# Optimization experiments

Hardware: AMD Instinct MI355X
Metric: run time of the kernel (lower is better)

The kernel has to match this reference:

```python
import jax, jax.numpy as jnp
import numpy as np

DIM = 256
RADIUS = 3
DIAM = 2 * RADIUS + 1          # 7
NNEIGH = DIAM * DIAM           # 49
B, H, W = 2, 64, 64
EPS_LN = 1e-6
EPS_NORM = 1e-7


def conv1x1(x, w, b):
    # x: [B,Cin,H,W], w: [Cout,Cin], b: [Cout]
    return jnp.einsum('oi,bihw->bohw', w, x) + b[None, :, None, None]


def layernorm2d(x, g, b):
    # channel-wise norm as in LayerNorm2d (mean/var over channel dim)
    u = x.mean(1, keepdims=True)
    s = ((x - u) ** 2).mean(1, keepdims=True)
    xn = (x - u) / jnp.sqrt(s + EPS_LN)
    return g[None, :, None, None] * xn + b[None, :, None, None]


def unfold_reflect(x, r):
    # torch F.unfold(pad(x, reflect, r), kernel=2r+1).reshape(B,C,D*D,H,W)
    d = 2 * r + 1
    hh, ww = x.shape[2], x.shape[3]
    xp = jnp.pad(x, ((0, 0), (0, 0), (r, r), (r, r)), mode='reflect')
    pats = [xp[:, :, i:i + hh, j:j + ww] for i in range(d) for j in range(d)]
    return jnp.stack(pats, axis=2)  # [B,C,D*D,H,W]


def setup_inputs() -> dict:
    key = jax.random.key(0)
    ks = jax.random.split(key, 20)
    sc_c = 1.0 / np.sqrt(DIM)
    sc_f = 1.0 / np.sqrt(NNEIGH + DIM)
    inp = {
        'spatial_feats': jax.random.normal(ks[0], (B, DIM, H, W), jnp.float32),
        'semantic_feats': jax.random.normal(ks[1], (B, DIM, H, W), jnp.float32),
        # range_proj: conv1x1 -> LN2d -> SiLU -> conv1x1
        'rp_w1': jax.random.normal(ks[2], (DIM, DIM), jnp.float32) * sc_c,
        'rp_b1': jnp.zeros((DIM,), jnp.float32),
        'rp_g': jnp.ones((DIM,), jnp.float32),
        'rp_be': jnp.zeros((DIM,), jnp.float32),
        'rp_w2': jax.random.normal(ks[3], (DIM, DIM), jnp.float32) * sc_c,
        'rp_b2': jnp.zeros((DIM,), jnp.float32),
        # fixup_proj: conv1x1(49+C->49) -> LN2d -> SiLU -> conv1x1(49->49)
        'fp_w1': jax.random.normal(ks[4], (NNEIGH, NNEIGH + DIM), jnp.float32) * sc_f,
        'fp_b1': jnp.zeros((NNEIGH,), jnp.float32),
        'fp_g': jnp.ones((NNEIGH,), jnp.float32),
        'fp_be': jnp.zeros((NNEIGH,), jnp.float32),
        'fp_w2': jax.random.normal(ks[5], (NNEIGH, NNEIGH), jnp.float32) * (1.0 / np.sqrt(NNEIGH)),
        'fp_b2': jnp.zeros((NNEIGH,), jnp.float32),
        # output_proj: conv1x1 -> LN2d -> conv1x1
        'op_w1': jax.random.normal(ks[6], (DIM, DIM), jnp.float32) * sc_c,
        'op_b1': jnp.zeros((DIM,), jnp.float32),
        'op_g': jnp.ones((DIM,), jnp.float32),
        'op_be': jnp.zeros((DIM,), jnp.float32),
        'op_w2': jax.random.normal(ks[7], (DIM, DIM), jnp.float32) * sc_c,
        'op_b2': jnp.zeros((DIM,), jnp.float32),
        'sigma_spatial': jnp.ones((), jnp.float32),
    }
    return inp


def reference(spatial_feats, semantic_feats,
              rp_w1, rp_b1, rp_g, rp_be, rp_w2, rp_b2,
              fp_w1, fp_b1, fp_g, fp_be, fp_w2, fp_b2,
              op_w1, op_b1, op_g, op_be, op_w2, op_b2,
              sigma_spatial):
    scale = jnp.asarray(DIM ** 0.5, spatial_feats.dtype)
    # range_proj(semantic_feats)
    px = conv1x1(semantic_feats, rp_w1, rp_b1)
    px = jax.nn.silu(layernorm2d(px, rp_g, rp_be))
    px = conv1x1(px, rp_w2, rp_b2)  # [B,C,H,W]

    # spatial (Gaussian) kernel over the window
    lin = jnp.linspace(-1.0, 1.0, DIAM)
    xg, yg = jnp.meshgrid(lin, lin, indexing='ij')
    spatial_kernel = jnp.exp(-(xg ** 2 + yg ** 2) / (2.0 * sigma_spatial ** 2))
    spatial_kernel = spatial_kernel.reshape(1, NNEIGH, 1, 1)

    # range kernel: local similarity + softmax over the 49 neighbors
    queries = unfold_reflect(px, RADIUS)                       # [B,C,N,H,W]
    sim = jnp.einsum('bcnhw,bchw->bnhw', queries, px) / scale
    range_kernel = jax.nn.softmax(sim.astype(jnp.float32), axis=1).astype(px.dtype)

    # neighborhoods of spatial features
    neighborhoods = unfold_reflect(spatial_feats, RADIUS)      # [B,C,N,H,W]

    # gated fixup correction
    ck = range_kernel * spatial_kernel                          # [B,N,H,W]
    fx = conv1x1(jnp.concatenate([ck, semantic_feats], axis=1), fp_w1, fp_b1)
    fx = jax.nn.silu(layernorm2d(fx, fp_g, fp_be))
    fx = conv1x1(fx, fp_w2, fp_b2)
    ck = ck + ck * jax.nn.sigmoid(fx)
    ck = ck / (ck.sum(1, keepdims=True) + EPS_NORM)

    # weighted neighborhood sum
    out = jnp.einsum('bcnhw,bnhw->bchw', neighborhoods, ck)

    # output_proj (note: no SiLU here, matching the module)
    out = conv1x1(out, op_w1, op_b1)
    out = layernorm2d(out, op_g, op_be)
    out = conv1x1(out, op_w2, op_b2)
    return out
```

## Files before the change

kernel.cpp:

```cpp
#include <hip/hip_runtime.h>
#include <cstdint>

#define HW 4096
#define C_ 256
#define NN 49
#define KW 305

typedef __bf16 bf16;
typedef bf16 bf16x8 __attribute__((ext_vector_type(8)));
typedef bf16 bf16x4 __attribute__((ext_vector_type(4)));
typedef float f32x4 __attribute__((ext_vector_type(4)));

#define GLD16(src, dst) __builtin_amdgcn_global_load_lds( \
    (const __attribute__((address_space(1))) uint32_t*)(src), \
    (__attribute__((address_space(3))) uint32_t*)(dst), 16, 0, 0)

__device__ __forceinline__ int refl(int i) { return i < 0 ? -i : (i > 63 ? 126 - i : i); }
__device__ __forceinline__ float sigmoidf_(float x) { return 1.f / (1.f + __expf(-x)); }

__global__ __launch_bounds__(256) void setup_k(const float* __restrict__ spatial,
                                               const float* __restrict__ semantic,
                                               const float* __restrict__ rp_w1,
                                               const float* __restrict__ rp_w2,
                                               const float* __restrict__ op_w1,
                                               const float* __restrict__ op_w2,
                                               const float* __restrict__ fp_w1,
                                               const float* __restrict__ fp_w2,
                                               const float* __restrict__ sigma,
                                               bf16* __restrict__ spb, bf16* __restrict__ seb,
                                               bf16* __restrict__ wrp1, bf16* __restrict__ wrp2,
                                               bf16* __restrict__ wop1, bf16* __restrict__ wop2,
                                               bf16* __restrict__ w1ckb, bf16* __restrict__ w1sb,
                                               bf16* __restrict__ w2Tg, float* __restrict__ sk)
{
    __shared__ float tile[32][33];
    const int bid = blockIdx.x, t = threadIdx.x;
    if (bid < 4096) {
        int z = bid >> 10, r = bid & 1023;
        int b = z & 1;
        const float* src = (z >> 1) ? semantic : spatial;
        bf16* dst = (z >> 1) ? seb : spb;
        int p0 = (r & 127) * 32, c0 = (r >> 7) * 32;
        int tx = t & 31, ty = t >> 5;
        const float* s = src + (size_t)b * C_ * HW;
        #pragma unroll
        for (int i = 0; i < 32; i += 8)
            tile[ty + i][tx] = s[(size_t)(c0 + ty + i) * HW + p0 + tx];
        __syncthreads();
        int p = t >> 3, cq = (t & 7) * 4;
        bf16x4 o = {(bf16)tile[cq][p], (bf16)tile[cq + 1][p], (bf16)tile[cq + 2][p], (bf16)tile[cq + 3][p]};
        *(bf16x4*)&dst[((size_t)b * HW + p0 + p) * C_ + c0 + cq] = o;
        return;
    }
    int pid = bid - 4096;
    if (pid < 256) {
        const float* src = (pid < 64) ? rp_w1 : (pid < 128) ? rp_w2 : (pid < 192) ? op_w1 : op_w2;
        bf16* dst = (pid < 64) ? wrp1 : (pid < 128) ? wrp2 : (pid < 192) ? wop1 : wop2;
        int i = ((pid & 63) * 256 + t) * 4;
        f32x4 v = *(const f32x4*)&src[i];
        bf16x4 o = {(bf16)v[0], (bf16)v[1], (bf16)v[2], (bf16)v[3]};
        *(bf16x4*)&dst[i] = o;
    } else if (pid == 256) {
        if (t < NN) {
            int i = t / 7, j = t % 7;
            float xg = (i - 3) * (1.f / 3.f), yg = (j - 3) * (1.f / 3.f);
            float s = sigma[0];
            sk[t] = __expf(-(xg * xg + yg * yg) / (2.f * s * s));
        }
    } else if (pid < 270) {
        int idx = (pid - 257) * 256 + t;
        if (idx < NN * 64) {
            int k = idx >> 6, o = idx & 63;
            w1ckb[idx] = (o < NN) ? (bf16)fp_w1[o * KW + k] : (bf16)0.f;
        }
    } else if (pid < 334) {
        int idx = (pid - 270) * 256 + t;
        int o = idx >> 8, c = idx & 255;
        w1sb[idx] = (o < NN) ? (bf16)fp_w1[o * KW + NN + c] : (bf16)0.f;
    } else {
        int idx = (pid - 334) * 256 + t;
        if (idx < NN * 64) {
            int k = idx >> 6, o = idx & 63;
            w2Tg[idx] = (o < NN) ? (bf16)fp_w2[o * NN + k] : (bf16)0.f;
        }
    }
}

__device__ __forceinline__ void stage_b(const bf16* __restrict__ Wp, bf16* dst, int kc, int t)
{
    const bf16* gB = Wp + (size_t)(t >> 2) * C_ + kc + (((t & 3) ^ ((t >> 3) & 3)) * 8);
    #pragma unroll
    for (int ii = 0; ii < 4; ++ii)
        GLD16(gB + (size_t)ii * 64 * C_, dst + ii * 2048 + t * 8);
}

template<bool SILU, int MODE>
__global__ __launch_bounds__(256) void conv_pair(const bf16* __restrict__ X,
                                                 const bf16* __restrict__ W1,
                                                 const float* __restrict__ b1v,
                                                 const float* __restrict__ g,
                                                 const float* __restrict__ be,
                                                 const bf16* __restrict__ W2,
                                                 const float* __restrict__ b2v,
                                                 void* __restrict__ Yv)
{
    __shared__ __align__(16) bf16 Xf[32 * 256];
    __shared__ __align__(16) bf16 Mid[32 * 256];
    __shared__ __align__(16) bf16 Bs[2][256 * 32];
    __shared__ float lnred[32][4][2];
    const int t = threadIdx.x;
    const int lane = t & 63, wc = t >> 6;
    const int l15 = lane & 15, kb = lane >> 4;
    const long q0 = (long)blockIdx.x * 32;

    {
        const int r8 = t >> 5, slot = t & 31;
        const bf16* gX = X + (q0 + r8) * C_ + ((slot ^ (r8 & 7)) * 8);
        #pragma unroll
        for (int i = 0; i < 4; ++i)
            GLD16(gX + (size_t)i * 8 * C_, &Xf[i * 2048 + t * 8]);
    }
    stage_b(W1, &Bs[0][0], 0, t);

    const int x7 = l15 & 7;
    const int bsl = (kb ^ ((l15 >> 1) & 3)) * 8;
    int boff[4];
    #pragma unroll
    for (int n = 0; n < 4; ++n)
        boff[n] = (wc * 64 + n * 16 + l15) * 32 + bsl;
    const int a0base = l15 * 256;
    const int a1base = (16 + l15) * 256;

    f32x4 acc[2][4];
    #pragma unroll
    for (int m = 0; m < 2; ++m)
        #pragma unroll
        for (int n = 0; n < 4; ++n) acc[m][n] = (f32x4){0.f, 0.f, 0.f, 0.f};

    __syncthreads();
    int cur = 0;
    #pragma unroll
    for (int ks = 0; ks < 8; ++ks) {
        if (ks < 7) stage_b(W1, &Bs[cur ^ 1][0], (ks + 1) * 32, t);
        const int ko = ((ks * 4 + kb) ^ x7) * 8;
        bf16x8 a0 = *(const bf16x8*)&Xf[a0base + ko];
        bf16x8 a1 = *(const bf16x8*)&Xf[a1base + ko];
        #pragma unroll
        for (int n = 0; n < 4; ++n) {
            bf16x8 b = *(const bf16x8*)&Bs[cur][boff[n]];
            acc[0][n] = __builtin_amdgcn_mfma_f32_16x16x32_bf16(a0, b, acc[0][n], 0, 0, 0);
            acc[1][n] = __builtin_amdgcn_mfma_f32_16x16x32_bf16(a1, b, acc[1][n], 0, 0, 0);
        }
        __syncthreads();
        cur ^= 1;
    }

    stage_b(W2, &Bs[0][0], 0, t);

    float s4[2][4], ss4[2][4];
    #pragma unroll
    for (int m = 0; m < 2; ++m)
        #pragma unroll
        for (int r = 0; r < 4; ++r) { s4[m][r] = 0.f; ss4[m][r] = 0.f; }
    #pragma unroll
    for (int n = 0; n < 4; ++n) {
        float bo = b1v[wc * 64 + n * 16 + l15];
        #pragma unroll
        for (int m = 0; m < 2; ++m)
            #pragma unroll
            for (int r = 0; r < 4; ++r) {
                float v = acc[m][n][r] + bo;
                acc[m][n][r] = v;
                s4[m][r] += v; ss4[m][r] += v * v;
            }
    }
    #pragma unroll
    for (int off = 1; off <= 8; off <<= 1)
        #pragma unroll
        for (int m = 0; m < 2; ++m)
            #pragma unroll
            for (int r = 0; r < 4; ++r) {
                s4[m][r]  += __shfl_xor(s4[m][r], off, 64);
                ss4[m][r] += __shfl_xor(ss4[m][r], off, 64);
            }
    if (l15 == 0) {
        #pragma unroll
        for (int m = 0; m < 2; ++m)
            #pragma unroll
            for (int r = 0; r < 4; ++r) {
                lnred[m * 16 + kb * 4 + r][wc][0] = s4[m][r];
                lnred[m * 16 + kb * 4 + r][wc][1] = ss4[m][r];
            }
    }
    __syncthreads();
    float mean[2][4], rstd[2][4];
    #pragma unroll
    for (int m = 0; m < 2; ++m)
        #pragma unroll
        for (int r = 0; r < 4; ++r) {
            int p = m * 16 + kb * 4 + r;
            float st  = lnred[p][0][0] + lnred[p][1][0] + lnred[p][2][0] + lnred[p][3][0];
            float sst = lnred[p][0][1] + lnred[p][1][1] + lnred[p][2][1] + lnred[p][3][1];
            mean[m][r] = st * (1.f / 256.f);
            float var = sst * (1.f / 256.f) - mean[m][r] * mean[m][r];
            rstd[m][r] = rsqrtf(var + 1e-6f);
        }
    #pragma unroll
    for (int n = 0; n < 4; ++n) {
        int ch = wc * 64 + n * 16 + l15;
        float gv = g[ch], bev = be[ch];
        #pragma unroll
        for (int m = 0; m < 2; ++m)
            #pragma unroll
            for (int r = 0; r < 4; ++r) {
                float y = (acc[m][n][r] - mean[m][r]) * rstd[m][r] * gv + bev;
                if (SILU) y *= sigmoidf_(y);
                int p = m * 16 + kb * 4 + r;
                Mid[p * 256 + (((ch >> 3) ^ (p & 7)) * 8) + (ch & 7)] = (bf16)y;
            }
    }
    __syncthreads();

    f32x4 acc2[2][4];
    #pragma unroll
    for (int m = 0; m < 2; ++m)
        #pragma unroll
        for (int n = 0; n < 4; ++n) acc2[m][n] = (f32x4){0.f, 0.f, 0.f, 0.f};
    cur = 0;
    #pragma unroll
    for (int ks = 0; ks < 8; ++ks) {
        if (ks < 7) stage_b(W2, &Bs[cur ^ 1][0], (ks + 1) * 32, t);
        const int ko = ((ks * 4 + kb) ^ x7) * 8;
        bf16x8 a0 = *(const bf16x8*)&Mid[a0base + ko];
        bf16x8 a1 = *(const bf16x8*)&Mid[a1base + ko];
        #pragma unroll
        for (int n = 0; n < 4; ++n) {
            bf16x8 b = *(const bf16x8*)&Bs[cur][boff[n]];
            acc2[0][n] = __builtin_amdgcn_mfma_f32_16x16x32_bf16(a0, b, acc2[0][n], 0, 0, 0);
            acc2[1][n] = __builtin_amdgcn_mfma_f32_16x16x32_bf16(a1, b, acc2[1][n], 0, 0, 0);
        }
        __syncthreads();
        cur ^= 1;
    }

    if constexpr (MODE == 0) {
        #pragma unroll
        for (int n = 0; n < 4; ++n) {
            int ch = wc * 64 + n * 16 + l15;
            float bo = b2v[ch];
            #pragma unroll
            for (int m = 0; m < 2; ++m)
                #pragma unroll
                for (int r = 0; r < 4; ++r)
                    Xf[(m * 16 + kb * 4 + r) * 256 + ch] = (bf16)(acc2[m][n][r] + bo);
        }
        __syncthreads();
        bf16* Y = (bf16*)Yv;
        const int p = t >> 3, cb = (t & 7) * 32;
        #pragma unroll
        for (int i = 0; i < 4; ++i) {
            bf16x8 v = *(const bf16x8*)&Xf[p * 256 + cb + i * 8];
            *(bf16x8*)&Y[(q0 + p) * C_ + cb + i * 8] = v;
        }
    } else {
        float* Y = (float*)Yv;
        const int bb = (int)(q0 >> 12);
        #pragma unroll
        for (int n = 0; n < 4; ++n) {
            int ch = wc * 64 + n * 16 + l15;
            float bo = b2v[ch];
            #pragma unroll
            for (int m = 0; m < 2; ++m) {
                int pp = (int)(q0 & 4095) + m * 16 + kb * 4;
                f32x4 val = {acc2[m][n][0] + bo, acc2[m][n][1] + bo,
                             acc2[m][n][2] + bo, acc2[m][n][3] + bo};
                *(f32x4*)&Y[((size_t)bb * C_ + ch) * HW + pp] = val;
            }
        }
    }
}

__global__ __launch_bounds__(256) void attn_out_k(const bf16* __restrict__ px,
                                                  const bf16* __restrict__ spb,
                                                  const bf16* __restrict__ seb,
                                                  const bf16* __restrict__ w1sb,
                                                  const bf16* __restrict__ w1ckb,
                                                  const bf16* __restrict__ w2Tg,
                                                  const float* __restrict__ b1,
                                                  const float* __restrict__ b2,
                                                  const float* __restrict__ g,
                                                  const float* __restrict__ be,
                                                  const float* __restrict__ sk,
                                                  const bf16* __restrict__ wop1,
                                                  const float* __restrict__ ob1,
                                                  const float* __restrict__ og,
                                                  const float* __restrict__ obe,
                                                  const bf16* __restrict__ wop2,
                                                  const float* __restrict__ ob2,
                                                  float* __restrict__ Y)
{
    __shared__ __align__(16) char shm[72768];
    bf16*  uni = (bf16*)(shm);
    float* ckl = (float*)(shm + 51200);
    float* hb  = (float*)(shm + 55360);
    float* S   = (float*)(shm + 56384);
    float* fxs = (float*)(shm + 64000);
    bf16*  Bs0 = (bf16*)(shm + 56384);
    bf16*  Bs1 = (bf16*)(shm + 16384);
    bf16*  Xg  = (bf16*)(shm);
    bf16*  Mid = (bf16*)(shm + 32768);
    float* lnred = (float*)(shm + 40960);

    const int t = threadIdx.x, lane = t & 63, wid = t >> 6;
    const int l15 = lane & 15, kb = lane >> 4, l31 = lane & 31;
    const int blk = blockIdx.x;
    const int batch = blk >> 8, tt = blk & 255;
    const int h0 = (tt >> 4) * 4, w0 = (tt & 15) * 4;
    const long base = (long)batch * HW;

    const float bo  = (lane < NN) ? b1[lane] : 0.f;
    const float gl  = (lane < NN) ? g[lane] : 0.f;
    const float bel = (lane < NN) ? be[lane] : 0.f;
    const float b2l = (lane < NN) ? b2[lane] : 0.f;
    const float skv = (lane < NN) ? sk[lane] : 0.f;
    const int nn_ = (lane < NN) ? lane : 0;
    const int dy = nn_ / 7, dx = nn_ % 7;

    #pragma unroll
    for (int i = 0; i < 13; ++i) {
        int st = i * 256 + t;
        if (st < 3200) {
            int u = st >> 5, s = st & 31;
            int uy = (u * 205) >> 11, ux = u - uy * 10;
            long grow = base + refl(h0 + uy - 3) * 64 + refl(w0 + ux - 3);
            GLD16(spb + grow * C_ + s * 8, &uni[u * 256 + s * 8]);
        }
    }

    const int ppy = l15 >> 2, ppx = l15 & 3;
    const long qB = base + (h0 + ppy) * 64 + (w0 + ppx);
    const bf16* bpxp = px + qB * C_ + kb * 8;
    const bf16* bsemp = seb + qB * C_ + kb * 8;

    bool valid[3], ispx[3];
    const bf16* arow[3];
    #pragma unroll
    for (int j = 0; j < 3; ++j) {
        int tid = wid + 4 * j;
        valid[j] = tid < 11;
        ispx[j] = tid < 7;
        int u = tid * 16 + l15;
        int uy = (u * 205) >> 11, ux = u - uy * 10;
        long grow = (u < 100) ? base + refl(h0 + uy - 3) * 64 + refl(w0 + ux - 3) : base;
        int o = ((tid - 7) & 3) * 16 + l15;
        arow[j] = ispx[j] ? (px + grow * C_ + kb * 8)
                          : (w1sb + (size_t)o * C_ + kb * 8);
    }

    f32x4 acc[3];
    #pragma unroll
    for (int j = 0; j < 3; ++j) acc[j] = (f32x4){0.f, 0.f, 0.f, 0.f};

    #pragma unroll
    for (int ks = 0; ks < 8; ++ks) {
        bf16x8 bp = *(const bf16x8*)(bpxp + ks * 32);
        bf16x8 bs = *(const bf16x8*)(bsemp + ks * 32);
        #pragma unroll
        for (int j = 0; j < 3; ++j) {
            if (valid[j]) {
                bf16x8 a = *(const bf16x8*)(arow[j] + ks * 32);
                acc[j] = __builtin_amdgcn_mfma_f32_16x16x32_bf16(a, ispx[j] ? bp : bs, acc[j], 0, 0, 0);
            }
        }
    }

    float w1r[NN], w2r[NN];
    #pragma unroll
    for (int k = 0; k < NN; ++k) {
        w1r[k] = (float)w1ckb[k * 64 + lane];
        w2r[k] = (float)w2Tg[k * 64 + lane];
    }

    #pragma unroll
    for (int j = 0; j < 3; ++j) {
        if (valid[j]) {
            int tid = wid + 4 * j;
            float* dst = ispx[j] ? &S[(tid * 16 + kb * 4) * 17 + l15]
                                 : &fxs[(((tid - 7) * 16) + kb * 4) * 17 + l15];
            dst[0] = acc[j][0]; dst[17] = acc[j][1]; dst[34] = acc[j][2]; dst[51] = acc[j][3];
        }
    }
    __syncthreads();

    #pragma unroll
    for (int j = 0; j < 4; ++j) {
        int p = wid * 4 + j, py = p >> 2, px4 = p & 3;
        int u = (py + dy) * 10 + px4 + dx;
        float sval = (lane < NN) ? S[u * 17 + p] * 0.0625f : -1e30f;
        float mx = sval;
        #pragma unroll
        for (int off = 32; off; off >>= 1) mx = fmaxf(mx, __shfl_xor(mx, off, 64));
        float ev = (lane < NN) ? __expf(sval - mx) : 0.f;
        float ssum = ev;
        #pragma unroll
        for (int off = 32; off; off >>= 1) ssum += __shfl_xor(ssum, off, 64);
        ckl[p * 65 + lane] = (lane < NN) ? (ev / ssum) * skv : 0.f;
    }

    #pragma unroll
    for (int j = 0; j < 4; ++j) {
        int p = wid * 4 + j;
        float fxa = 0.f, fxb = 0.f;
        #pragma unroll
        for (int k = 0; k < 48; k += 2) {
            fxa += w1r[k] * ckl[p * 65 + k];
            fxb += w1r[k + 1] * ckl[p * 65 + k + 1];
        }
        fxa += w1r[48] * ckl[p * 65 + 48];
        float fx = fxs[lane * 17 + p] + bo + fxa + fxb;
        float s = fx, ss = fx * fx;
        #pragma unroll
        for (int off = 32; off; off >>= 1) {
            s  += __shfl_xor(s, off, 64);
            ss += __shfl_xor(ss, off, 64);
        }
        float mean = s * (1.f / 49.f);
        float var  = ss * (1.f / 49.f) - mean * mean;
        float rstd = rsqrtf(var + 1e-6f);
        float hv = 0.f;
        if (lane < NN) {
            float xn = (fx - mean) * rstd * gl + bel;
            hv = xn * sigmoidf_(xn);
        }
        hb[wid * 64 + lane] = hv;
        float ckv = 0.f;
        if (lane < NN) {
            float ca = 0.f, cb = 0.f;
            #pragma unroll
            for (int k = 0; k < 48; k += 2) {
                ca += w2r[k] * hb[wid * 64 + k];
                cb += w2r[k + 1] * hb[wid * 64 + k + 1];
            }
            ca += w2r[48] * hb[wid * 64 + 48];
            ckv = ckl[p * 65 + lane] * (1.f + sigmoidf_(b2l + ca + cb));
        }
        float tot = ckv;
        #pragma unroll
        for (int off = 32; off; off >>= 1) tot += __shfl_xor(tot, off, 64);
        ckl[p * 65 + lane] = (lane < NN) ? ckv / (tot + 1e-7f) : 0.f;
    }
    __syncthreads();

    stage_b(wop1, Bs0, 0, t);

    bf16x8 ov[2];
    #pragma unroll
    for (int j = 0; j < 2; ++j) {
        const int gp = wid * 4 + j * 2 + (lane >> 5);
        const int ub = (gp >> 2) * 10 + (gp & 3);
        float a[8];
        #pragma unroll
        for (int e = 0; e < 8; ++e) a[e] = 0.f;
        #pragma unroll
        for (int dyy = 0; dyy < 7; ++dyy) {
            bf16x8 v[7];
            #pragma unroll
            for (int dxx = 0; dxx < 7; ++dxx) {
                int u = ub + dyy * 10 + dxx;
                v[dxx] = *(const bf16x8*)&uni[u * 256 + l31 * 8];
            }
            #pragma unroll
            for (int dxx = 0; dxx < 7; ++dxx) {
                float cv = ckl[gp * 65 + dyy * 7 + dxx];
                #pragma unroll
                for (int e = 0; e < 8; ++e) a[e] += cv * (float)v[dxx][e];
            }
        }
        #pragma unroll
        for (int e = 0; e < 8; ++e) ov[j][e] = (bf16)a[e];
    }
    __syncthreads();

    #pragma unroll
    for (int j = 0; j < 2; ++j) {
        const int gp = wid * 4 + j * 2 + (lane >> 5);
        *(bf16x8*)&Xg[gp * 256 + ((l31 ^ (gp & 7)) * 8)] = ov[j];
    }
    __syncthreads();

    const int x7 = l15 & 7;
    const int bsl = (kb ^ ((l15 >> 1) & 3)) * 8;
    int boff[4];
    #pragma unroll
    for (int n = 0; n < 4; ++n)
        boff[n] = (wid * 64 + n * 16 + l15) * 32 + bsl;

    f32x4 cacc[4];
    #pragma unroll
    for (int n = 0; n < 4; ++n) cacc[n] = (f32x4){0.f, 0.f, 0.f, 0.f};

    int cur = 0;
    #pragma unroll
    for (int ks = 0; ks < 8; ++ks) {
        if (ks < 7) stage_b(wop1, cur ? Bs0 : Bs1, (ks + 1) * 32, t);
        const int ko = ((ks * 4 + kb) ^ x7) * 8;
        bf16x8 a = *(const bf16x8*)&Xg[l15 * 256 + ko];
        #pragma unroll
        for (int n = 0; n < 4; ++n) {
            bf16x8 b = *(const bf16x8*)&((cur ? Bs1 : Bs0)[boff[n]]);
            cacc[n] = __builtin_amdgcn_mfma_f32_16x16x32_bf16(a, b, cacc[n], 0, 0, 0);
        }
        __syncthreads();
        cur ^= 1;
    }

    stage_b(wop2, Bs0, 0, t);

    float s4[4] = {0.f, 0.f, 0.f, 0.f}, ss4[4] = {0.f, 0.f, 0.f, 0.f};
    #pragma unroll
    for (int n = 0; n < 4; ++n) {
        float bv = ob1[wid * 64 + n * 16 + l15];
        #pragma unroll
        for (int r = 0; r < 4; ++r) {
            float v = cacc[n][r] + bv;
            cacc[n][r] = v;
            s4[r] += v; ss4[r] += v * v;
        }
    }
    #pragma unroll
    for (int off = 1; off <= 8; off <<= 1)
        #pragma unroll
        for (int r = 0; r < 4; ++r) {
            s4[r]  += __shfl_xor(s4[r], off, 64);
            ss4[r] += __shfl_xor(ss4[r], off, 64);
        }
    if (l15 == 0) {
        #pragma unroll
        for (int r = 0; r < 4; ++r) {
            lnred[((kb * 4 + r) * 4 + wid) * 2 + 0] = s4[r];
            lnred[((kb * 4 + r) * 4 + wid) * 2 + 1] = ss4[r];
        }
    }
    __syncthreads();
    float mean[4], rstd[4];
    #pragma unroll
    for (int r = 0; r < 4; ++r) {
        int p = kb * 4 + r;
        float st  = lnred[(p * 4 + 0) * 2] + lnred[(p * 4 + 1) * 2] + lnred[(p * 4 + 2) * 2] + lnred[(p * 4 + 3) * 2];
        float sst = lnred[(p * 4 + 0) * 2 + 1] + lnred[(p * 4 + 1) * 2 + 1] + lnred[(p * 4 + 2) * 2 + 1] + lnred[(p * 4 + 3) * 2 + 1];
        mean[r] = st * (1.f / 256.f);
        float var = sst * (1.f / 256.f) - mean[r] * mean[r];
        rstd[r] = rsqrtf(var + 1e-6f);
    }
    #pragma unroll
    for (int n = 0; n < 4; ++n) {
        int ch = wid * 64 + n * 16 + l15;
        float gv = og[ch], bev = obe[ch];
        #pragma unroll
        for (int r = 0; r < 4; ++r) {
            float y = (cacc[n][r] - mean[r]) * rstd[r] * gv + bev;
            int p = kb * 4 + r;
            Mid[p * 256 + (((ch >> 3) ^ (p & 7)) * 8) + (ch & 7)] = (bf16)y;
        }
    }
    __syncthreads();

    f32x4 cacc2[4];
    #pragma unroll
    for (int n = 0; n < 4; ++n) cacc2[n] = (f32x4){0.f, 0.f, 0.f, 0.f};
    cur = 0;
    #pragma unroll
    for (int ks = 0; ks < 8; ++ks) {
        if (ks < 7) stage_b(wop2, cur ? Bs0 : Bs1, (ks + 1) * 32, t);
        const int ko = ((ks * 4 + kb) ^ x7) * 8;
        bf16x8 a = *(const bf16x8*)&Mid[l15 * 256 + ko];
        #pragma unroll
        for (int n = 0; n < 4; ++n) {
            bf16x8 b = *(const bf16x8*)&((cur ? Bs1 : Bs0)[boff[n]]);
            cacc2[n] = __builtin_amdgcn_mfma_f32_16x16x32_bf16(a, b, cacc2[n], 0, 0, 0);
        }
        __syncthreads();
        cur ^= 1;
    }

    {
        const size_t rowbase = ((size_t)batch * C_) * HW + (size_t)(h0 + kb) * 64 + w0;
        #pragma unroll
        for (int n = 0; n < 4; ++n) {
            int ch = wid * 64 + n * 16 + l15;
            float bv = ob2[ch];
            f32x4 val = {cacc2[n][0] + bv, cacc2[n][1] + bv, cacc2[n][2] + bv, cacc2[n][3] + bv};
            *(f32x4*)&Y[rowbase + (size_t)ch * HW] = val;
        }
    }
}

extern "C" void kernel_launch(void* const* d_in, const int* in_sizes, int n_in,
                              void* d_out, int out_size, void* d_ws, size_t ws_size,
                              hipStream_t stream)
{
    const float* spatial  = (const float*)d_in[0];
    const float* semantic = (const float*)d_in[1];
    const float* rp_w1 = (const float*)d_in[2];
    const float* rp_b1 = (const float*)d_in[3];
    const float* rp_g  = (const float*)d_in[4];
    const float* rp_be = (const float*)d_in[5];
    const float* rp_w2 = (const float*)d_in[6];
    const float* rp_b2 = (const float*)d_in[7];
    const float* fp_w1 = (const float*)d_in[8];
    const float* fp_b1 = (const float*)d_in[9];
    const float* fp_g  = (const float*)d_in[10];
    const float* fp_be = (const float*)d_in[11];
    const float* fp_w2 = (const float*)d_in[12];
    const float* fp_b2 = (const float*)d_in[13];
    const float* op_w1 = (const float*)d_in[14];
    const float* op_b1 = (const float*)d_in[15];
    const float* op_g  = (const float*)d_in[16];
    const float* op_be = (const float*)d_in[17];
    const float* op_w2 = (const float*)d_in[18];
    const float* op_b2 = (const float*)d_in[19];
    const float* sigma = (const float*)d_in[20];

    const size_t NPX = 2 * (size_t)HW;
    float* ws = (float*)d_ws;
    float* sk    = ws;
    bf16* bfbase = (bf16*)(sk + 64);
    bf16* spb = bfbase;
    bf16* seb = spb + NPX * C_;
    bf16* t1  = seb + NPX * C_;
    bf16* wrp1 = t1 + NPX * C_;
    bf16* wrp2 = wrp1 + C_ * C_;
    bf16* wop1 = wrp2 + C_ * C_;
    bf16* wop2 = wop1 + C_ * C_;
    bf16* w1sb = wop2 + C_ * C_;
    bf16* w2Tg = w1sb + 64 * C_;
    bf16* w1ckb = w2Tg + 3200;

    setup_k<<<4443, 256, 0, stream>>>(spatial, semantic, rp_w1, rp_w2, op_w1, op_w2,
                                      fp_w1, fp_w2, sigma,
                                      spb, seb, wrp1, wrp2, wop1, wop2,
                                      w1ckb, w1sb, w2Tg, sk);

    conv_pair<true, 0><<<256, 256, 0, stream>>>(seb, wrp1, rp_b1, rp_g, rp_be, wrp2, rp_b2, t1);

    attn_out_k<<<512, 256, 0, stream>>>(t1, spb, seb, w1sb, w1ckb, w2Tg, fp_b1, fp_b2,
                                        fp_g, fp_be, sk,
                                        wop1, op_b1, op_g, op_be, wop2, op_b2,
                                        (float*)d_out);
}
```

Before: 64.86 us.

## Load GEMM weight fragments directly from global memory, halve conv_pair tile

Removes the double-buffered LDS staging of weight tiles (stage_b with global_load_lds) in both conv_pair and attn_out_k. Each lane now reads its bf16x8 weight fragment straight from global/L2, which also drops the per-k-step __syncthreads. conv_pair is shrunk to 16 pixels per block with twice as many blocks, and shared memory use falls in both kernels, which may allow more blocks per CU. The cost is more global/L2 traffic and latency exposed on the weight loads with no explicit prefetch, and in conv_pair each weight is reused across only 16 pixels instead of 32.

```diff
diff --git a/kernel.cpp b/kernel.cpp
--- a/kernel.cpp
+++ b/kernel.cpp
@@ -86,14 +86,6 @@
     }
 }
 
-__device__ __forceinline__ void stage_b(const bf16* __restrict__ Wp, bf16* dst, int kc, int t)
-{
-    const bf16* gB = Wp + (size_t)(t >> 2) * C_ + kc + (((t & 3) ^ ((t >> 3) & 3)) * 8);
-    #pragma unroll
-    for (int ii = 0; ii < 4; ++ii)
-        GLD16(gB + (size_t)ii * 64 * C_, dst + ii * 2048 + t * 8);
-}
-
 template<bool SILU, int MODE>
 __global__ __launch_bounds__(256) void conv_pair(const bf16* __restrict__ X,
                                                  const bf16* __restrict__ W1,
@@ -104,143 +96,104 @@
                                                  const float* __restrict__ b2v,
                                                  void* __restrict__ Yv)
 {
-    __shared__ __align__(16) bf16 Xf[32 * 256];
-    __shared__ __align__(16) bf16 Mid[32 * 256];
-    __shared__ __align__(16) bf16 Bs[2][256 * 32];
-    __shared__ float lnred[32][4][2];
+    __shared__ __align__(16) bf16 Xf[16 * 256];
+    __shared__ __align__(16) bf16 Mid[16 * 256];
+    __shared__ float lnred[16][4][2];
     const int t = threadIdx.x;
     const int lane = t & 63, wc = t >> 6;
     const int l15 = lane & 15, kb = lane >> 4;
-    const long q0 = (long)blockIdx.x * 32;
+    const long q0 = (long)blockIdx.x * 16;
 
     {
-        const int r8 = t >> 5, slot = t & 31;
-        const bf16* gX = X + (q0 + r8) * C_ + ((slot ^ (r8 & 7)) * 8);
-        #pragma unroll
-        for (int i = 0; i < 4; ++i)
-            GLD16(gX + (size_t)i * 8 * C_, &Xf[i * 2048 + t * 8]);
-    }
-    stage_b(W1, &Bs[0][0], 0, t);
+        const int row = t >> 5, slot = t & 31;
+        const bf16* gX = X + (q0 + row) * C_ + ((slot ^ (row & 7)) * 8);
+        GLD16(gX, &Xf[t * 8]);
+        GLD16(gX + 8 * C_, &Xf[2048 + t * 8]);
+    }
 
     const int x7 = l15 & 7;
-    const int bsl = (kb ^ ((l15 >> 1) & 3)) * 8;
-    int boff[4];
-    #pragma unroll
-    for (int n = 0; n < 4; ++n)
-        boff[n] = (wc * 64 + n * 16 + l15) * 32 + bsl;
-    const int a0base = l15 * 256;
-    const int a1base = (16 + l15) * 256;
-
-    f32x4 acc[2][4];
-    #pragma unroll
-    for (int m = 0; m < 2; ++m)
-        #pragma unroll
-        for (int n = 0; n < 4; ++n) acc[m][n] = (f32x4){0.f, 0.f, 0.f, 0.f};
-
-    __syncthreads();
-    int cur = 0;
+    const bf16* wb1 = W1 + (size_t)(wc * 64 + l15) * C_ + kb * 8;
+    const bf16* wb2 = W2 + (size_t)(wc * 64 + l15) * C_ + kb * 8;
+
+    f32x4 acc[4];
+    #pragma unroll
+    for (int n = 0; n < 4; ++n) acc[n] = (f32x4){0.f, 0.f, 0.f, 0.f};
+
+    __syncthreads();
+
     #pragma unroll
     for (int ks = 0; ks < 8; ++ks) {
-        if (ks < 7) stage_b(W1, &Bs[cur ^ 1][0], (ks + 1) * 32, t);
         const int ko = ((ks * 4 + kb) ^ x7) * 8;
-        bf16x8 a0 = *(const bf16x8*)&Xf[a0base + ko];
-        bf16x8 a1 = *(const bf16x8*)&Xf[a1base + ko];
-        #pragma unroll
-        for (int n = 0; n < 4; ++n) {
-            bf16x8 b = *(const bf16x8*)&Bs[cur][boff[n]];
-            acc[0][n] = __builtin_amdgcn_mfma_f32_16x16x32_bf16(a0, b, acc[0][n], 0, 0, 0);
-            acc[1][n] = __builtin_amdgcn_mfma_f32_16x16x32_bf16(a1, b, acc[1][n], 0, 0, 0);
-        }
-        __syncthreads();
-        cur ^= 1;
-    }
-
-    stage_b(W2, &Bs[0][0], 0, t);
-
-    float s4[2][4], ss4[2][4];
-    #pragma unroll
-    for (int m = 0; m < 2; ++m)
-        #pragma unroll
-        for (int r = 0; r < 4; ++r) { s4[m][r] = 0.f; ss4[m][r] = 0.f; }
+        bf16x8 a = *(const bf16x8*)&Xf[l15 * 256 + ko];
+        #pragma unroll
+        for (int n = 0; n < 4; ++n) {
+            bf16x8 b = *(const bf16x8*)(wb1 + (size_t)n * 16 * C_ + ks * 32);
+            acc[n] = __builtin_amdgcn_mfma_f32_16x16x32_bf16(a, b, acc[n], 0, 0, 0);
+        }
+    }
+
+    float s4[4] = {0.f, 0.f, 0.f, 0.f}, ss4[4] = {0.f, 0.f, 0.f, 0.f};
     #pragma unroll
     for (int n = 0; n < 4; ++n) {
         float bo = b1v[wc * 64 + n * 16 + l15];
         #pragma unroll
-        for (int m = 0; m < 2; ++m)
-            #pragma unroll
-            for (int r = 0; r < 4; ++r) {
-                float v = acc[m][n][r] + bo;
-                acc[m][n][r] = v;
-                s4[m][r] += v; ss4[m][r] += v * v;
-            }
+        for (int r = 0; r < 4; ++r) {
+            float v = acc[n][r] + bo;
+            acc[n][r] = v;
+            s4[r] += v; ss4[r] += v * v;
+        }
     }
     #pragma unroll
     for (int off = 1; off <= 8; off <<= 1)
         #pragma unroll
-        for (int m = 0; m < 2; ++m)
-            #pragma unroll
-            for (int r = 0; r < 4; ++r) {
-                s4[m][r]  += __shfl_xor(s4[m][r], off, 64);
-                ss4[m][r] += __shfl_xor(ss4[m][r], off, 64);
-            }
+        for (int r = 0; r < 4; ++r) {
+            s4[r]  += __shfl_xor(s4[r], off, 64);
+            ss4[r] += __shfl_xor(ss4[r], off, 64);
+        }
     if (l15 == 0) {
         #pragma unroll
-        for (int m = 0; m < 2; ++m)
-            #pragma unroll
-            for (int r = 0; r < 4; ++r) {
-                lnred[m * 16 + kb * 4 + r][wc][0] = s4[m][r];
-                lnred[m * 16 + kb * 4 + r][wc][1] = ss4[m][r];
-            }
-    }
-    __syncthreads();
-    float mean[2][4], rstd[2][4];
-    #pragma unroll
-    for (int m = 0; m < 2; ++m)
-        #pragma unroll
-        for (int r = 0; r < 4; ++r) {
-            int p = m * 16 + kb * 4 + r;
-            float st  = lnred[p][0][0] + lnred[p][1][0] + lnred[p][2][0] + lnred[p][3][0];
-            float sst = lnred[p][0][1] + lnred[p][1][1] + lnred[p][2][1] + lnred[p][3][1];
-            mean[m][r] = st * (1.f / 256.f);
-            float var = sst * (1.f / 256.f) - mean[m][r] * mean[m][r];
-            rstd[m][r] = rsqrtf(var + 1e-6f);
-        }
+        for (int r = 0; r < 4; ++r) {
+            lnred[kb * 4 + r][wc][0] = s4[r];
+            lnred[kb * 4 + r][wc][1] = ss4[r];
+        }
+    }
+    __syncthreads();
+    float mean[4], rstd[4];
+    #pragma unroll
+    for (int r = 0; r < 4; ++r) {
+        int p = kb * 4 + r;
+        float st  = lnred[p][0][0] + lnred[p][1][0] + lnred[p][2][0] + lnred[p][3][0];
+        float sst = lnred[p][0][1] + lnred[p][1][1] + lnred[p][2][1] + lnred[p][3][1];
+        mean[r] = st * (1.f / 256.f);
+        float var = sst * (1.f / 256.f) - mean[r] * mean[r];
+        rstd[r] = rsqrtf(var + 1e-6f);
+    }
     #pragma unroll
     for (int n = 0; n < 4; ++n) {
         int ch = wc * 64 + n * 16 + l15;
         float gv = g[ch], bev = be[ch];
         #pragma unroll
-        for (int m = 0; m < 2; ++m)
-            #pragma unroll
-            for (int r = 0; r < 4; ++r) {
-                float y = (acc[m][n][r] - mean[m][r]) * rstd[m][r] * gv + bev;
-                if (SILU) y *= sigmoidf_(y);
-                int p = m * 16 + kb * 4 + r;
-                Mid[p * 256 + (((ch >> 3) ^ (p & 7)) * 8) + (ch & 7)] = (bf16)y;
-            }
-    }
-    __syncthreads();
-
-    f32x4 acc2[2][4];
-    #pragma unroll
-    for (int m = 0; m < 2; ++m)
-        #pragma unroll
-        for (int n = 0; n < 4; ++n) acc2[m][n] = (f32x4){0.f, 0.f, 0.f, 0.f};
-    cur = 0;
+        for (int r = 0; r < 4; ++r) {
+            float y = (acc[n][r] - mean[r]) * rstd[r] * gv + bev;
+            if (SILU) y *= sigmoidf_(y);
+            int p = kb * 4 + r;
+            Mid[p * 256 + (((ch >> 3) ^ (p & 7)) * 8) + (ch & 7)] = (bf16)y;
+        }
+    }
+    __syncthreads();
+
+    f32x4 acc2[4];
+    #pragma unroll
+    for (int n = 0; n < 4; ++n) acc2[n] = (f32x4){0.f, 0.f, 0.f, 0.f};
     #pragma unroll
     for (int ks = 0; ks < 8; ++ks) {
-        if (ks < 7) stage_b(W2, &Bs[cur ^ 1][0], (ks + 1) * 32, t);
         const int ko = ((ks * 4 + kb) ^ x7) * 8;
-        bf16x8 a0 = *(const bf16x8*)&Mid[a0base + ko];
-        bf16x8 a1 = *(const bf16x8*)&Mid[a1base + ko];
-        #pragma unroll
-        for (int n = 0; n < 4; ++n) {
-            bf16x8 b = *(const bf16x8*)&Bs[cur][boff[n]];
-            acc2[0][n] = __builtin_amdgcn_mfma_f32_16x16x32_bf16(a0, b, acc2[0][n], 0, 0, 0);
-            acc2[1][n] = __builtin_amdgcn_mfma_f32_16x16x32_bf16(a1, b, acc2[1][n], 0, 0, 0);
-        }
-        __syncthreads();
-        cur ^= 1;
+        bf16x8 a = *(const bf16x8*)&Mid[l15 * 256 + ko];
+        #pragma unroll
+        for (int n = 0; n < 4; ++n) {
+            bf16x8 b = *(const bf16x8*)(wb2 + (size_t)n * 16 * C_ + ks * 32);
+            acc2[n] = __builtin_amdgcn_mfma_f32_16x16x32_bf16(a, b, acc2[n], 0, 0, 0);
+        }
     }
 
     if constexpr (MODE == 0) {
@@ -249,33 +202,26 @@
             int ch = wc * 64 + n * 16 + l15;
             float bo = b2v[ch];
             #pragma unroll
-            for (int m = 0; m < 2; ++m)
-                #pragma unroll
-                for (int r = 0; r < 4; ++r)
-                    Xf[(m * 16 + kb * 4 + r) * 256 + ch] = (bf16)(acc2[m][n][r] + bo);
+            for (int r = 0; r < 4; ++r)
+                Xf[(kb * 4 + r) * 256 + ch] = (bf16)(acc2[n][r] + bo);
         }
         __syncthreads();
         bf16* Y = (bf16*)Yv;
-        const int p = t >> 3, cb = (t & 7) * 32;
-        #pragma unroll
-        for (int i = 0; i < 4; ++i) {
-            bf16x8 v = *(const bf16x8*)&Xf[p * 256 + cb + i * 8];
-            *(bf16x8*)&Y[(q0 + p) * C_ + cb + i * 8] = v;
-        }
+        const int p = t >> 4, cb = (t & 15) * 16;
+        bf16x8 v0 = *(const bf16x8*)&Xf[p * 256 + cb];
+        bf16x8 v1 = *(const bf16x8*)&Xf[p * 256 + cb + 8];
+        *(bf16x8*)&Y[(q0 + p) * C_ + cb] = v0;
+        *(bf16x8*)&Y[(q0 + p) * C_ + cb + 8] = v1;
     } else {
         float* Y = (float*)Yv;
         const int bb = (int)(q0 >> 12);
+        const int pp = (int)(q0 & 4095) + kb * 4;
         #pragma unroll
         for (int n = 0; n < 4; ++n) {
             int ch = wc * 64 + n * 16 + l15;
             float bo = b2v[ch];
-            #pragma unroll
-            for (int m = 0; m < 2; ++m) {
-                int pp = (int)(q0 & 4095) + m * 16 + kb * 4;
-                f32x4 val = {acc2[m][n][0] + bo, acc2[m][n][1] + bo,
-                             acc2[m][n][2] + bo, acc2[m][n][3] + bo};
-                *(f32x4*)&Y[((size_t)bb * C_ + ch) * HW + pp] = val;
-            }
+            f32x4 val = {acc2[n][0] + bo, acc2[n][1] + bo, acc2[n][2] + bo, acc2[n][3] + bo};
+            *(f32x4*)&Y[((size_t)bb * C_ + ch) * HW + pp] = val;
         }
     }
 }
@@ -299,17 +245,15 @@
                                                   const float* __restrict__ ob2,
                                                   float* __restrict__ Y)
 {
-    __shared__ __align__(16) char shm[72768];
+    __shared__ __align__(16) char shm[68352];
     bf16*  uni = (bf16*)(shm);
     float* ckl = (float*)(shm + 51200);
     float* hb  = (float*)(shm + 55360);
     float* S   = (float*)(shm + 56384);
     float* fxs = (float*)(shm + 64000);
-    bf16*  Bs0 = (bf16*)(shm + 56384);
-    bf16*  Bs1 = (bf16*)(shm + 16384);
     bf16*  Xg  = (bf16*)(shm);
-    bf16*  Mid = (bf16*)(shm + 32768);
-    float* lnred = (float*)(shm + 40960);
+    bf16*  Mid = (bf16*)(shm + 16384);
+    float* lnred = (float*)(shm + 32768);
 
     const int t = threadIdx.x, lane = t & 63, wid = t >> 6;
     const int l15 = lane & 15, kb = lane >> 4, l31 = lane & 31;
@@ -449,9 +393,6 @@
         for (int off = 32; off; off >>= 1) tot += __shfl_xor(tot, off, 64);
         ckl[p * 65 + lane] = (lane < NN) ? ckv / (tot + 1e-7f) : 0.f;
     }
-    __syncthreads();
-
-    stage_b(wop1, Bs0, 0, t);
 
     bf16x8 ov[2];
     #pragma unroll
@@ -489,32 +430,23 @@
     __syncthreads();
 
     const int x7 = l15 & 7;
-    const int bsl = (kb ^ ((l15 >> 1) & 3)) * 8;
-    int boff[4];
-    #pragma unroll
-    for (int n = 0; n < 4; ++n)
-        boff[n] = (wid * 64 + n * 16 + l15) * 32 + bsl;
+    const bf16* wb1 = wop1 + (size_t)(wid * 64 + l15) * C_ + kb * 8;
+    const bf16* wb2 = wop2 + (size_t)(wid * 64 + l15) * C_ + kb * 8;
 
     f32x4 cacc[4];
     #pragma unroll
     for (int n = 0; n < 4; ++n) cacc[n] = (f32x4){0.f, 0.f, 0.f, 0.f};
 
-    int cur = 0;
     #pragma unroll
     for (int ks = 0; ks < 8; ++ks) {
-        if (ks < 7) stage_b(wop1, cur ? Bs0 : Bs1, (ks + 1) * 32, t);
         const int ko = ((ks * 4 + kb) ^ x7) * 8;
         bf16x8 a = *(const bf16x8*)&Xg[l15 * 256 + ko];
         #pragma unroll
         for (int n = 0; n < 4; ++n) {
-            bf16x8 b = *(const bf16x8*)&((cur ? Bs1 : Bs0)[boff[n]]);
+            bf16x8 b = *(const bf16x8*)(wb1 + (size_t)n * 16 * C_ + ks * 32);
             cacc[n] = __builtin_amdgcn_mfma_f32_16x16x32_bf16(a, b, cacc[n], 0, 0, 0);
         }
-        __syncthreads();
-        cur ^= 1;
-    }
-
-    stage_b(wop2, Bs0, 0, t);
+    }
 
     float s4[4] = {0.f, 0.f, 0.f, 0.f}, ss4[4] = {0.f, 0.f, 0.f, 0.f};
     #pragma unroll
@@ -568,19 +500,15 @@
     f32x4 cacc2[4];
     #pragma unroll
     for (int n = 0; n < 4; ++n) cacc2[n] = (f32x4){0.f, 0.f, 0.f, 0.f};
-    cur = 0;
     #pragma unroll
     for (int ks = 0; ks < 8; ++ks) {
-        if (ks < 7) stage_b(wop2, cur ? Bs0 : Bs1, (ks + 1) * 32, t);
         const int ko = ((ks * 4 + kb) ^ x7) * 8;
         bf16x8 a = *(const bf16x8*)&Mid[l15 * 256 + ko];
         #pragma unroll
         for (int n = 0; n < 4; ++n) {
-            bf16x8 b = *(const bf16x8*)&((cur ? Bs1 : Bs0)[boff[n]]);
+            bf16x8 b = *(const bf16x8*)(wb2 + (size_t)n * 16 * C_ + ks * 32);
             cacc2[n] = __builtin_amdgcn_mfma_f32_16x16x32_bf16(a, b, cacc2[n], 0, 0, 0);
         }
-        __syncthreads();
-        cur ^= 1;
     }
 
     {
@@ -641,7 +569,7 @@
                                       spb, seb, wrp1, wrp2, wop1, wop2,
                                       w1ckb, w1sb, w2Tg, sk);
 
-    conv_pair<true, 0><<<256, 256, 0, stream>>>(seb, wrp1, rp_b1, rp_g, rp_be, wrp2, rp_b2, t1);
+    conv_pair<true, 0><<<512, 256, 0, stream>>>(seb, wrp1, rp_b1, rp_g, rp_be, wrp2, rp_b2, t1);
 
     attn_out_k<<<512, 256, 0, stream>>>(t1, spb, seb, w1sb, w1ckb, w2Tg, fp_b1, fp_b2,
                                         fp_g, fp_be, sk,
```

Result: slower. 73.29 us (+13.0%).

## Halve attention tile to 2x4 pixels, double grid, read output weights from global

Applied to the files above, without the earlier changes.

The fused attention/output kernel now handles a 2x4 pixel tile instead of 4x4. That doubles the grid to 1024 blocks and cuts shared memory from about 72KB to about 49KB, aiming for more occupancy and better spread across CUs. The LDS double-buffered staging of the output-projection weights is removed. The MFMA B operands are loaded straight from global/L2, which drops the per-step barriers. The cost is half-empty MFMA tiles: rows 8-15 are zero-padded, so MFMA work per pixel doubles, the halo overlap gets worse, and weight reads from global are repeated per block.

```diff
diff --git a/kernel.cpp b/kernel.cpp
--- a/kernel.cpp
+++ b/kernel.cpp
@@ -299,23 +299,21 @@
                                                   const float* __restrict__ ob2,
                                                   float* __restrict__ Y)
 {
-    __shared__ __align__(16) char shm[72768];
+    __shared__ __align__(16) char shm[49248];
     bf16*  uni = (bf16*)(shm);
-    float* ckl = (float*)(shm + 51200);
-    float* hb  = (float*)(shm + 55360);
-    float* S   = (float*)(shm + 56384);
-    float* fxs = (float*)(shm + 64000);
-    bf16*  Bs0 = (bf16*)(shm + 56384);
-    bf16*  Bs1 = (bf16*)(shm + 16384);
+    float* ckl = (float*)(shm + 40960);
+    float* hb  = (float*)(shm + 43040);
+    float* S   = (float*)(shm + 44064);
+    float* fxs = (float*)(shm + 46944);
     bf16*  Xg  = (bf16*)(shm);
-    bf16*  Mid = (bf16*)(shm + 32768);
-    float* lnred = (float*)(shm + 40960);
+    bf16*  Mid = (bf16*)(shm + 8192);
+    float* lnred = (float*)(shm + 16384);
 
     const int t = threadIdx.x, lane = t & 63, wid = t >> 6;
     const int l15 = lane & 15, kb = lane >> 4, l31 = lane & 31;
     const int blk = blockIdx.x;
-    const int batch = blk >> 8, tt = blk & 255;
-    const int h0 = (tt >> 4) * 4, w0 = (tt & 15) * 4;
+    const int batch = blk >> 9, tt = blk & 511;
+    const int h0 = (tt >> 4) * 2, w0 = (tt & 15) * 4;
     const long base = (long)batch * HW;
 
     const float bo  = (lane < NN) ? b1[lane] : 0.f;
@@ -327,9 +325,9 @@
     const int dy = nn_ / 7, dx = nn_ % 7;
 
     #pragma unroll
-    for (int i = 0; i < 13; ++i) {
+    for (int i = 0; i < 10; ++i) {
         int st = i * 256 + t;
-        if (st < 3200) {
+        if (st < 2560) {
             int u = st >> 5, s = st & 31;
             int uy = (u * 205) >> 11, ux = u - uy * 10;
             long grow = base + refl(h0 + uy - 3) * 64 + refl(w0 + ux - 3);
@@ -337,7 +335,7 @@
         }
     }
 
-    const int ppy = l15 >> 2, ppx = l15 & 3;
+    const int ppy = (l15 >> 2) & 1, ppx = l15 & 3;
     const long qB = base + (h0 + ppy) * 64 + (w0 + ppx);
     const bf16* bpxp = px + qB * C_ + kb * 8;
     const bf16* bsemp = seb + qB * C_ + kb * 8;
@@ -347,12 +345,12 @@
     #pragma unroll
     for (int j = 0; j < 3; ++j) {
         int tid = wid + 4 * j;
-        valid[j] = tid < 11;
-        ispx[j] = tid < 7;
+        valid[j] = tid < 9;
+        ispx[j] = tid < 5;
         int u = tid * 16 + l15;
         int uy = (u * 205) >> 11, ux = u - uy * 10;
-        long grow = (u < 100) ? base + refl(h0 + uy - 3) * 64 + refl(w0 + ux - 3) : base;
-        int o = ((tid - 7) & 3) * 16 + l15;
+        long grow = (u < 80) ? base + refl(h0 + uy - 3) * 64 + refl(w0 + ux - 3) : base;
+        int o = ((tid - 5) & 3) * 16 + l15;
         arow[j] = ispx[j] ? (px + grow * C_ + kb * 8)
                           : (w1sb + (size_t)o * C_ + kb * 8);
     }
@@ -383,20 +381,20 @@
 
     #pragma unroll
     for (int j = 0; j < 3; ++j) {
-        if (valid[j]) {
+        if (valid[j] && l15 < 8) {
             int tid = wid + 4 * j;
-            float* dst = ispx[j] ? &S[(tid * 16 + kb * 4) * 17 + l15]
-                                 : &fxs[(((tid - 7) * 16) + kb * 4) * 17 + l15];
-            dst[0] = acc[j][0]; dst[17] = acc[j][1]; dst[34] = acc[j][2]; dst[51] = acc[j][3];
-        }
-    }
-    __syncthreads();
-
-    #pragma unroll
-    for (int j = 0; j < 4; ++j) {
-        int p = wid * 4 + j, py = p >> 2, px4 = p & 3;
+            float* dst = ispx[j] ? &S[(tid * 16 + kb * 4) * 9 + l15]
+                                 : &fxs[(((tid - 5) * 16) + kb * 4) * 9 + l15];
+            dst[0] = acc[j][0]; dst[9] = acc[j][1]; dst[18] = acc[j][2]; dst[27] = acc[j][3];
+        }
+    }
+    __syncthreads();
+
+    #pragma unroll
+    for (int j = 0; j < 2; ++j) {
+        int p = wid * 2 + j, py = p >> 2, px4 = p & 3;
         int u = (py + dy) * 10 + px4 + dx;
-        float sval = (lane < NN) ? S[u * 17 + p] * 0.0625f : -1e30f;
+        float sval = (lane < NN) ? S[u * 9 + p] * 0.0625f : -1e30f;
         float mx = sval;
         #pragma unroll
         for (int off = 32; off; off >>= 1) mx = fmaxf(mx, __shfl_xor(mx, off, 64));
@@ -408,8 +406,8 @@
     }
 
     #pragma unroll
-    for (int j = 0; j < 4; ++j) {
-        int p = wid * 4 + j;
+    for (int j = 0; j < 2; ++j) {
+        int p = wid * 2 + j;
         float fxa = 0.f, fxb = 0.f;
         #pragma unroll
         for (int k = 0; k < 48; k += 2) {
@@ -417,7 +415,7 @@
             fxb += w1r[k + 1] * ckl[p * 65 + k + 1];
         }
         fxa += w1r[48] * ckl[p * 65 + 48];
-        float fx = fxs[lane * 17 + p] + bo + fxa + fxb;
+        float fx = fxs[lane * 9 + p] + bo + fxa + fxb;
         float s = fx, ss = fx * fx;
         #pragma unroll
         for (int off = 32; off; off >>= 1) {
@@ -449,14 +447,10 @@
         for (int off = 32; off; off >>= 1) tot += __shfl_xor(tot, off, 64);
         ckl[p * 65 + lane] = (lane < NN) ? ckv / (tot + 1e-7f) : 0.f;
     }
-    __syncthreads();
-
-    stage_b(wop1, Bs0, 0, t);
-
-    bf16x8 ov[2];
-    #pragma unroll
-    for (int j = 0; j < 2; ++j) {
-        const int gp = wid * 4 + j * 2 + (lane >> 5);
+
+    bf16x8 ov;
+    {
+        const int gp = wid * 2 + (lane >> 5);
         const int ub = (gp >> 2) * 10 + (gp & 3);
         float a[8];
         #pragma unroll
@@ -477,44 +471,36 @@
             }
         }
         #pragma unroll
-        for (int e = 0; e < 8; ++e) ov[j][e] = (bf16)a[e];
-    }
-    __syncthreads();
-
-    #pragma unroll
-    for (int j = 0; j < 2; ++j) {
-        const int gp = wid * 4 + j * 2 + (lane >> 5);
-        *(bf16x8*)&Xg[gp * 256 + ((l31 ^ (gp & 7)) * 8)] = ov[j];
+        for (int e = 0; e < 8; ++e) ov[e] = (bf16)a[e];
+    }
+    __syncthreads();
+
+    {
+        const int gp = wid * 2 + (lane >> 5);
+        *(bf16x8*)&Xg[gp * 256 + ((l31 ^ (gp & 7)) * 8)] = ov;
+        bf16x8 z = {};
+        *(bf16x8*)&Xg[(8 + (t >> 5)) * 256 + (t & 31) * 8] = z;
     }
     __syncthreads();
 
     const int x7 = l15 & 7;
-    const int bsl = (kb ^ ((l15 >> 1) & 3)) * 8;
-    int boff[4];
-    #pragma unroll
-    for (int n = 0; n < 4; ++n)
-        boff[n] = (wid * 64 + n * 16 + l15) * 32 + bsl;
+    const bf16* wb1 = wop1 + (size_t)(wid * 64 + l15) * C_ + kb * 8;
+    const bf16* wb2 = wop2 + (size_t)(wid * 64 + l15) * C_ + kb * 8;
 
     f32x4 cacc[4];
     #pragma unroll
     for (int n = 0; n < 4; ++n) cacc[n] = (f32x4){0.f, 0.f, 0.f, 0.f};
 
-    int cur = 0;
     #pragma unroll
     for (int ks = 0; ks < 8; ++ks) {
-        if (ks < 7) stage_b(wop1, cur ? Bs0 : Bs1, (ks + 1) * 32, t);
         const int ko = ((ks * 4 + kb) ^ x7) * 8;
         bf16x8 a = *(const bf16x8*)&Xg[l15 * 256 + ko];
         #pragma unroll
         for (int n = 0; n < 4; ++n) {
-            bf16x8 b = *(const bf16x8*)&((cur ? Bs1 : Bs0)[boff[n]]);
+            bf16x8 b = *(const bf16x8*)(wb1 + (size_t)n * 16 * C_ + ks * 32);
             cacc[n] = __builtin_amdgcn_mfma_f32_16x16x32_bf16(a, b, cacc[n], 0, 0, 0);
         }
-        __syncthreads();
-        cur ^= 1;
-    }
-
-    stage_b(wop2, Bs0, 0, t);
+    }
 
     float s4[4] = {0.f, 0.f, 0.f, 0.f}, ss4[4] = {0.f, 0.f, 0.f, 0.f};
     #pragma unroll
@@ -550,7 +536,7 @@
         float sst = lnred[(p * 4 + 0) * 2 + 1] + lnred[(p * 4 + 1) * 2 + 1] + lnred[(p * 4 + 2) * 2 + 1] + lnred[(p * 4 + 3) * 2 + 1];
         mean[r] = st * (1.f / 256.f);
         float var = sst * (1.f / 256.f) - mean[r] * mean[r];
-        rstd[r] = rsqrtf(var + 1e-6f);
+        rstd[r] = rsqrtf(fabsf(var) + 1e-6f);
     }
     #pragma unroll
     for (int n = 0; n < 4; ++n) {
@@ -568,22 +554,18 @@
     f32x4 cacc2[4];
     #pragma unroll
     for (int n = 0; n < 4; ++n) cacc2[n] = (f32x4){0.f, 0.f, 0.f, 0.f};
-    cur = 0;
     #pragma unroll
     for (int ks = 0; ks < 8; ++ks) {
-        if (ks < 7) stage_b(wop2, cur ? Bs0 : Bs1, (ks + 1) * 32, t);
         const int ko = ((ks * 4 + kb) ^ x7) * 8;
         bf16x8 a = *(const bf16x8*)&Mid[l15 * 256 + ko];
         #pragma unroll
         for (int n = 0; n < 4; ++n) {
-            bf16x8 b = *(const bf16x8*)&((cur ? Bs1 : Bs0)[boff[n]]);
+            bf16x8 b = *(const bf16x8*)(wb2 + (size_t)n * 16 * C_ + ks * 32);
             cacc2[n] = __builtin_amdgcn_mfma_f32_16x16x32_bf16(a, b, cacc2[n], 0, 0, 0);
         }
-        __syncthreads();
-        cur ^= 1;
-    }
-
-    {
+    }
+
+    if (kb < 2) {
         const size_t rowbase = ((size_t)batch * C_) * HW + (size_t)(h0 + kb) * 64 + w0;
         #pragma unroll
         for (int n = 0; n < 4; ++n) {
@@ -643,8 +625,8 @@
 
     conv_pair<true, 0><<<256, 256, 0, stream>>>(seb, wrp1, rp_b1, rp_g, rp_be, wrp2, rp_b2, t1);
 
-    attn_out_k<<<512, 256, 0, stream>>>(t1, spb, seb, w1sb, w1ckb, w2Tg, fp_b1, fp_b2,
-                                        fp_g, fp_be, sk,
-                                        wop1, op_b1, op_g, op_be, wop2, op_b2,
-                                        (float*)d_out);
+    attn_out_k<<<1024, 256, 0, stream>>>(t1, spb, seb, w1sb, w1ckb, w2Tg, fp_b1, fp_b2,
+                                         fp_g, fp_be, sk,
+                                         wop1, op_b1, op_g, op_be, wop2, op_b2,
+                                         (float*)d_out);
 }
```

Result: slower. 91.66 us (+41.3%).
